# Optimization experiments

Hardware: AMD Instinct MI355X
Metric: run time of the kernel (lower is better)

## Reference

```python
import jax, jax.numpy as jnp
import numpy as np

BATCH = 4
N1 = 131072   # stage-1 voxels (total over batch)
N2 = 32768    # stage-2 (stride-2 downsampled) voxels
D_MODEL = 128
D_INNER = 2 * D_MODEL
D_STATE = 16
D_CONV = 4
DT_RANK = 8   # ceil(d_model / 16)
EPS = 1e-5


def _ln(x, g, b):
    mu = x.mean(-1, keepdims=True)
    v = ((x - mu) ** 2).mean(-1, keepdims=True)
    return (x - mu) * jax.lax.rsqrt(v + EPS) * g + b


def _causal_conv(x, w, b):
    # x: [B,L,Di], w: [Di,K] -> depthwise causal conv1d
    y = jax.lax.conv_general_dilated(
        x.transpose(0, 2, 1), w[:, None, :], (1,), [(D_CONV - 1, 0)],
        dimension_numbers=('NCH', 'OIH', 'NCH'), feature_group_count=D_INNER)
    return y.transpose(0, 2, 1) + b


def _mamba_block(x, ln_g, ln_b, in_w, conv_w, conv_b, xproj_w, dtproj_w, dtproj_b, A_log, Dp, out_w):
    # create_block: LayerNorm -> Mamba mixer (selective scan); returns hidden states
    h = _ln(x, ln_g, ln_b)
    xz = h @ in_w.T                          # [B,L,2*Di]
    xc, z = jnp.split(xz, 2, axis=-1)
    xc = jax.nn.silu(_causal_conv(xc, conv_w, conv_b))
    dbl = xc @ xproj_w.T                     # [B,L,dt_rank+2*d_state]
    dt = jax.nn.softplus(dbl[..., :DT_RANK] @ dtproj_w.T + dtproj_b)  # [B,L,Di]
    Bm = dbl[..., DT_RANK:DT_RANK + D_STATE]
    Cm = dbl[..., DT_RANK + D_STATE:]
    A = -jnp.exp(A_log)                      # [Di,ds]

    def step(hst, inp):
        dt_t, b_t, c_t, u_t = inp            # [B,Di],[B,ds],[B,ds],[B,Di]
        hst = jnp.exp(dt_t[..., None] * A) * hst + (dt_t * u_t)[..., None] * b_t[:, None, :]
        return hst, jnp.einsum('bds,bs->bd', hst, c_t)

    h0 = jnp.zeros((x.shape[0], D_INNER, D_STATE), x.dtype)
    xs = (dt.transpose(1, 0, 2), Bm.transpose(1, 0, 2), Cm.transpose(1, 0, 2), xc.transpose(1, 0, 2))
    _, ys = jax.lax.scan(step, h0, xs)       # ys: [L,B,Di]
    y = ys.transpose(1, 0, 2) + xc * Dp
    y = y * jax.nn.silu(z)
    return y @ out_w.T


def _mamba_params(key):
    ks = jax.random.split(key, 6)
    s = lambda k, sh, sc: jax.random.normal(k, sh, jnp.float32) * sc
    return dict(
        ln_g=jnp.ones((D_MODEL,), jnp.float32), ln_b=jnp.zeros((D_MODEL,), jnp.float32),
        in_w=s(ks[0], (2 * D_INNER, D_MODEL), 0.05),
        conv_w=s(ks[1], (D_INNER, D_CONV), 0.2), conv_b=jnp.zeros((D_INNER,), jnp.float32),
        xproj_w=s(ks[2], (DT_RANK + 2 * D_STATE, D_INNER), 0.05),
        dtproj_w=s(ks[3], (D_INNER, DT_RANK), 0.1), dtproj_b=s(ks[4], (D_INNER,), 0.1),
        A_log=jnp.log(jnp.tile(jnp.arange(1, D_STATE + 1, dtype=jnp.float32), (D_INNER, 1))),
        D=jnp.ones((D_INNER,), jnp.float32),
        out_w=s(ks[5], (D_MODEL, D_INNER), 0.05))


def setup_inputs():
    key = jax.random.key(0)
    k = jax.random.split(key, 10)
    inp = {
        'feats_s1': jax.random.normal(k[0], (N1, D_MODEL), jnp.float32),
        'feats_s2': jax.random.normal(k[1], (N2, D_MODEL), jnp.float32),
        'pos_s1': jax.random.uniform(k[2], (N1, 3), jnp.float32),
        'pos_s2': jax.random.uniform(k[3], (N2, 3), jnp.float32),
        'hilbert_s1': jax.random.randint(k[4], (N1,), 0, 1 << 30, jnp.int32),
        'hilbert_s2': jax.random.randint(k[5], (N2,), 0, 1 << 30, jnp.int32),
        'pe_w': jax.random.normal(k[6], (D_MODEL, 3), jnp.float32) * 0.1,
        'pe_b': jnp.zeros((D_MODEL,), jnp.float32),
        'norm_g': jnp.ones((D_MODEL,), jnp.float32), 'norm_b': jnp.zeros((D_MODEL,), jnp.float32),
        'normb_g': jnp.ones((D_MODEL,), jnp.float32), 'normb_b': jnp.zeros((D_MODEL,), jnp.float32),
    }
    for pref, kk in (('m1_', k[7]), ('m2_', k[8])):
        for n, v in _mamba_params(kk).items():
            inp[pref + n] = v
    return inp


def _forward(feats_s1, feats_s2, pos_s1, pos_s2, pe_w, pe_b, norm_g, norm_b, normb_g, normb_b,
             m1_ln_g, m1_ln_b, m1_in_w, m1_conv_w, m1_conv_b, m1_xproj_w, m1_dtproj_w, m1_dtproj_b, m1_A_log, m1_D, m1_out_w,
             m2_ln_g, m2_ln_b, m2_in_w, m2_conv_w, m2_conv_b, m2_xproj_w, m2_dtproj_w, m2_dtproj_b, m2_A_log, m2_D, m2_out_w,
             hilbert_s1, hilbert_s2):
    L1, L2 = N1 // BATCH, N2 // BATCH
    m1 = (m1_ln_g, m1_ln_b, m1_in_w, m1_conv_w, m1_conv_b, m1_xproj_w, m1_dtproj_w, m1_dtproj_b, m1_A_log, m1_D, m1_out_w)
    m2 = (m2_ln_g, m2_ln_b, m2_in_w, m2_conv_w, m2_conv_b, m2_xproj_w, m2_dtproj_w, m2_dtproj_b, m2_A_log, m2_D, m2_out_w)

    # stage 2: hilbert-order forward scan through mamba_layer1
    f2 = (feats_s2 + pos_s2 @ pe_w.T + pe_b).reshape(BATCH, L2, D_MODEL)
    o2 = jnp.argsort(hilbert_s2.reshape(BATCH, L2), axis=-1)          # inds_curt_to_next
    seq2 = jnp.take_along_axis(f2, o2[..., None], axis=1)
    out2 = _mamba_block(seq2, *m1)
    back2 = jnp.take_along_axis(out2, jnp.argsort(o2, axis=-1)[..., None], axis=1).reshape(N2, D_MODEL)
    out_s2 = _ln(back2, norm_g, norm_b)

    # stage 1: flipped hilbert-order (backward) scan through mamba_layer2
    f1 = (feats_s1 + pos_s1 @ pe_w.T + pe_b).reshape(BATCH, L1, D_MODEL)
    o1 = jnp.argsort(hilbert_s1.reshape(BATCH, L1), axis=-1)
    seq1 = jnp.take_along_axis(f1, o1[..., None], axis=1)[:, ::-1, :]
    out1 = _mamba_block(seq1, *m2)[:, ::-1, :]
    back1 = jnp.take_along_axis(out1, jnp.argsort(o1, axis=-1)[..., None], axis=1).reshape(N1, D_MODEL)
    out_s1 = _ln(back1, normb_g, normb_b)

    return jnp.concatenate([out_s1, out_s2], axis=0)   # [N1+N2, d_model]


def reference(feats_s1, feats_s2, pos_s1, pos_s2, pe_w, pe_b, norm_g, norm_b, normb_g, normb_b,
              m1_ln_g, m1_ln_b, m1_in_w, m1_conv_w, m1_conv_b, m1_xproj_w, m1_dtproj_w, m1_dtproj_b, m1_A_log, m1_D, m1_out_w,
              m2_ln_g, m2_ln_b, m2_in_w, m2_conv_w, m2_conv_b, m2_xproj_w, m2_dtproj_w, m2_dtproj_b, m2_A_log, m2_D, m2_out_w,
              hilbert_s1, hilbert_s2):
    return _forward(feats_s1, feats_s2, pos_s1, pos_s2, pe_w, pe_b, norm_g, norm_b, normb_g, normb_b,
                    m1_ln_g, m1_ln_b, m1_in_w, m1_conv_w, m1_conv_b, m1_xproj_w, m1_dtproj_w, m1_dtproj_b, m1_A_log, m1_D, m1_out_w,
                    m2_ln_g, m2_ln_b, m2_in_w, m2_conv_w, m2_conv_b, m2_xproj_w, m2_dtproj_w, m2_dtproj_b, m2_A_log, m2_D, m2_out_w,
                    hilbert_s1, hilbert_s2)
```

## Files before the change

kernel.cpp:

```cpp
#include <hip/hip_runtime.h>
#include <hip/hip_bf16.h>

#define DEV __device__ __forceinline__

constexpr int BATCH_ = 4;
constexpr int N1_ = 131072;
constexpr int N2_ = 32768;
constexpr int L1_ = N1_ / BATCH_;
constexpr int L2_ = N2_ / BATCH_;
constexpr int DM_ = 128;
constexpr int DI_ = 256;
constexpr int DS_ = 16;
constexpr int DTR_ = 8;
constexpr int TOT_ = N1_ + N2_;

constexpr int TA_ = 32;
constexpr int TAH_ = TA_ + 3;
constexpr int NTILE1_ = L1_ / TA_;
constexpr int NTILE2_ = L2_ / TA_;
constexpr int NTILES_ = 4 * NTILE1_ + 4 * NTILE2_;

constexpr int TS_ = 128;
constexpr int NCH1_ = L1_ / TS_;
constexpr int NCH2_ = L2_ / TS_;
constexpr int NCHUNKS_ = 4 * NCH1_ + 4 * NCH2_;

constexpr int NST_ = 160;

constexpr int IN1_OFF = 0;
constexpr int IN2_OFF = 65536;
constexpr int XP1_OFF = 131072;
constexpr int XP2_OFF = 143360;
constexpr int OW1_OFF = 155648;
constexpr int OW2_OFF = 188416;
constexpr int W16_TOT = 221184;

typedef short short8 __attribute__((ext_vector_type(8)));
typedef float f32x4 __attribute__((ext_vector_type(4)));

struct MP {
  const float* ln_g; const float* ln_b; const float* in_w;
  const float* conv_w; const float* conv_b; const float* xproj_w;
  const float* dtproj_w; const float* dtproj_b; const float* A_log;
  const float* Dp; const float* out_w;
};

DEV float softplusf(float x) {
  return fmaxf(x, 0.f) + __logf(1.f + __expf(-fabsf(x)));
}

DEV unsigned short f2bf(float f) {
  unsigned u = __builtin_bit_cast(unsigned, f);
  u += 0x7fffu + ((u >> 16) & 1u);
  return (unsigned short)(u >> 16);
}
DEV float bf2f(unsigned short s) {
  unsigned u = ((unsigned)s) << 16;
  return __builtin_bit_cast(float, u);
}

DEV void sort_tile_info(int tile, int& seg, int& tis, int& slotbase) {
  if (tile < 128) { seg = tile >> 5; tis = tile & 31; slotbase = seg * L1_; }
  else { seg = 4 + ((tile - 128) >> 3); tis = (tile - 128) & 7; slotbase = N1_ + (seg - 4) * L2_; }
}

__global__ __launch_bounds__(256) void k_prep(
    const float* __restrict__ in_w1, const float* __restrict__ xp1,
    const float* __restrict__ ow1,
    const float* __restrict__ in_w2, const float* __restrict__ xp2,
    const float* __restrict__ ow2,
    unsigned short* __restrict__ w16)
{
  const int i = blockIdx.x * 256 + threadIdx.x;
  if (i >= W16_TOT) return;
  float v;
  if (i < IN2_OFF) v = in_w1[i - IN1_OFF];
  else if (i < XP1_OFF) v = in_w2[i - IN2_OFF];
  else if (i < XP2_OFF) {
    const int j = i - XP1_OFF; const int r = j >> 8;
    v = (r < 40) ? xp1[j] : 0.f;
  } else if (i < OW1_OFF) {
    const int j = i - XP2_OFF; const int r = j >> 8;
    v = (r < 40) ? xp2[j] : 0.f;
  } else if (i < OW2_OFF) v = ow1[i - OW1_OFF];
  else v = ow2[i - OW2_OFF];
  w16[i] = f2bf(v);
}

__global__ __launch_bounds__(256) void k_hist(
    const int* __restrict__ hil1, const int* __restrict__ hil2,
    const unsigned* __restrict__ ksrc, unsigned* __restrict__ histg,
    int shift, int pass0)
{
  const int tile = blockIdx.x;
  int seg, tis, slotbase;
  sort_tile_info(tile, seg, tis, slotbase);
  const int tid = threadIdx.x;
  __shared__ unsigned h[1024];
  #pragma unroll
  for (int i = 0; i < 4; ++i) h[i * 256 + tid] = 0;
  __syncthreads();
  #pragma unroll
  for (int it = 0; it < 4; ++it) {
    const int li = tis * 1024 + it * 256 + tid;
    unsigned k;
    if (pass0) k = (unsigned)(seg < 4 ? hil1[seg * L1_ + li] : hil2[(seg - 4) * L2_ + li]);
    else       k = ksrc[slotbase + li];
    atomicAdd(&h[(k >> shift) & 1023u], 1u);
  }
  __syncthreads();
  #pragma unroll
  for (int i = 0; i < 4; ++i)
    histg[tile * 1024 + i * 256 + tid] = h[i * 256 + tid];
}

__global__ __launch_bounds__(256) void k_scanoff(
    const unsigned* __restrict__ histg, unsigned* __restrict__ offg)
{
  const int seg = blockIdx.x;
  const int ntiles = seg < 4 ? 32 : 8;
  const int tilebase = seg < 4 ? seg * 32 : 128 + (seg - 4) * 8;
  const int tid = threadIdx.x;
  const int d0 = tid * 4;
  unsigned tot[4] = {0, 0, 0, 0};
  for (int t = 0; t < ntiles; ++t) {
    const unsigned* hp = &histg[(size_t)(tilebase + t) * 1024 + d0];
    tot[0] += hp[0]; tot[1] += hp[1]; tot[2] += hp[2]; tot[3] += hp[3];
  }
  unsigned lp[4]; unsigned s = 0;
  #pragma unroll
  for (int j = 0; j < 4; ++j) { lp[j] = s; s += tot[j]; }
  const int lane = tid & 63, wv = tid >> 6;
  unsigned inc = s;
  #pragma unroll
  for (int off = 1; off < 64; off <<= 1) {
    unsigned v = (unsigned)__shfl_up((int)inc, off, 64);
    if (lane >= off) inc += v;
  }
  __shared__ unsigned wsum[4];
  if (lane == 63) wsum[wv] = inc;
  __syncthreads();
  unsigned wbase = 0;
  for (int w = 0; w < 4; ++w) if (w < wv) wbase += wsum[w];
  const unsigned base = wbase + inc - s;
  #pragma unroll
  for (int j = 0; j < 4; ++j) {
    unsigned run = base + lp[j];
    for (int t = 0; t < ntiles; ++t) {
      offg[(size_t)(tilebase + t) * 1024 + d0 + j] = run;
      run += histg[(size_t)(tilebase + t) * 1024 + d0 + j];
    }
  }
}

__global__ __launch_bounds__(256) void k_scatter(
    const int* __restrict__ hil1, const int* __restrict__ hil2,
    const unsigned* __restrict__ ksrc, const int* __restrict__ isrc,
    const unsigned* __restrict__ offg,
    unsigned* __restrict__ kdst, int* __restrict__ idst,
    int* __restrict__ o_all, int shift, int pass0, int last)
{
  const int tile = blockIdx.x;
  int seg, tis, slotbase;
  sort_tile_info(tile, seg, tis, slotbase);
  const int tid = threadIdx.x;
  const int lane = tid & 63, wv = tid >> 6;
  __shared__ unsigned runb[1024];
  __shared__ unsigned wcnt[4 * 1024];
  #pragma unroll
  for (int i = 0; i < 4; ++i) runb[i * 256 + tid] = offg[(size_t)tile * 1024 + i * 256 + tid];
  #pragma unroll
  for (int it = 0; it < 4; ++it) {
    #pragma unroll
    for (int i = 0; i < 16; ++i) wcnt[i * 256 + tid] = 0;
    __syncthreads();
    const int li = tis * 1024 + it * 256 + tid;
    unsigned k; int v;
    if (pass0) {
      k = (unsigned)(seg < 4 ? hil1[seg * L1_ + li] : hil2[(seg - 4) * L2_ + li]);
      v = li;
    } else {
      k = ksrc[slotbase + li]; v = isrc[slotbase + li];
    }
    const unsigned d = (k >> shift) & 1023u;
    unsigned long long m = ~0ull;
    #pragma unroll
    for (int b = 0; b < 10; ++b) {
      const unsigned long long bb = __ballot((int)((d >> b) & 1u));
      m &= ((d >> b) & 1u) ? bb : ~bb;
    }
    const unsigned lrank = (unsigned)__popcll(m & ((1ull << lane) - 1ull));
    wcnt[wv * 1024 + d] = (unsigned)__popcll(m);
    __syncthreads();
    unsigned prior = runb[d];
    for (int w = 0; w < 3; ++w) if (w < wv) prior += wcnt[w * 1024 + d];
    const unsigned pos = prior + lrank;
    if (last) o_all[slotbase + pos] = v;
    else { kdst[slotbase + pos] = k; idst[slotbase + pos] = v; }
    __syncthreads();
    #pragma unroll
    for (int i = 0; i < 4; ++i) {
      const int dd = i * 256 + tid;
      runb[dd] += wcnt[dd] + wcnt[1024 + dd] + wcnt[2048 + dd] + wcnt[3072 + dd];
    }
    __syncthreads();
  }
}

constexpr int HF_ = 132;
constexpr int HB_ = 136;
constexpr int XB_ = 264;
constexpr int OFF_HFP = 18480;
constexpr int OFF_HB16 = 36960;
constexpr int SMEM_A = 50016;

__global__ __launch_bounds__(256) void k_phaseA(
    const float* __restrict__ feats1, const float* __restrict__ feats2,
    const float* __restrict__ pos1, const float* __restrict__ pos2,
    const float* __restrict__ pe_w, const float* __restrict__ pe_b,
    MP p1, MP p2, const int* __restrict__ o_all,
    const unsigned short* __restrict__ w16,
    __hip_bfloat16* __restrict__ xc_g, __hip_bfloat16* __restrict__ z_g,
    float* __restrict__ dbl_g)
{
  const int blk = blockIdx.x;
  bool is1; int b, tile;
  if (blk < 4 * NTILE1_) { is1 = true; b = blk / NTILE1_; tile = blk % NTILE1_; }
  else { const int r = blk - 4 * NTILE1_; is1 = false; b = r / NTILE2_; tile = r % NTILE2_; }
  const int L = is1 ? L1_ : L2_;
  const int slotbase = is1 ? b * L1_ : N1_ + b * L2_;
  const float* feats = is1 ? feats1 + (size_t)b * L1_ * DM_ : feats2 + (size_t)b * L2_ * DM_;
  const float* pos = is1 ? pos1 + (size_t)b * L1_ * 3 : pos2 + (size_t)b * L2_ * 3;
  const MP P = is1 ? p2 : p1;
  const unsigned short* iw16 = w16 + (is1 ? IN2_OFF : IN1_OFF);
  const unsigned short* xp16 = w16 + (is1 ? XP2_OFF : XP1_OFF);
  const bool rev = is1;
  const int t0 = tile * TA_;
  const int pstart = rev ? t0 : t0 - 3;
  const int lsh = rev ? 0 : 3;

  __shared__ char smem[SMEM_A];
  unsigned short* xcb16 = (unsigned short*)smem;
  float* hfp = (float*)(smem + OFF_HFP);
  unsigned short* xc16 = (unsigned short*)(smem + OFF_HFP);
  unsigned short* hb16 = (unsigned short*)(smem + OFF_HB16);

  const int tid = threadIdx.x;
  const int lane = tid & 63, wv = tid >> 6;
  const int l15 = lane & 15, quad = lane >> 4;

  {
    unsigned* hz = (unsigned*)hb16;
    for (int i = tid; i < 48 * HB_ / 2; i += 256) hz[i] = 0;
    const int c = tid & 127;
    const int half = tid >> 7;
    const float pw0 = pe_w[c * 3 + 0], pw1 = pe_w[c * 3 + 1], pw2 = pe_w[c * 3 + 2];
    const float pb = pe_b[c];
    for (int lt = half; lt < TAH_; lt += 2) {
      const int p = pstart + lt;
      if (p >= 0 && p < L) {
        const int orig = o_all[slotbase + p];
        const float* fr = feats + (size_t)orig * DM_;
        const float* pr = pos + (size_t)orig * 3;
        hfp[lt * HF_ + c] = fr[c] + pr[0] * pw0 + pr[1] * pw1 + pr[2] * pw2 + pb;
      }
    }
  }
  __syncthreads();
  {
    for (int lt = wv; lt < TAH_; lt += 4) {
      const int p = pstart + lt;
      if (p < 0 || p >= L) continue;
      float x0 = hfp[lt * HF_ + lane], x1 = hfp[lt * HF_ + lane + 64];
      float s = x0 + x1, q = x0 * x0 + x1 * x1;
      #pragma unroll
      for (int off = 32; off; off >>= 1) {
        s += __shfl_xor(s, off, 64);
        q += __shfl_xor(q, off, 64);
      }
      const float mu = s * (1.f / 128.f);
      const float rs = rsqrtf(q * (1.f / 128.f) - mu * mu + 1e-5f);
      hb16[lt * HB_ + lane]      = f2bf((x0 - mu) * rs * P.ln_g[lane]      + P.ln_b[lane]);
      hb16[lt * HB_ + lane + 64] = f2bf((x1 - mu) * rs * P.ln_g[lane + 64] + P.ln_b[lane + 64]);
    }
  }
  __syncthreads();
  {
    short8 afr[3][4];
    #pragma unroll
    for (int mt = 0; mt < 3; ++mt)
      #pragma unroll
      for (int t = 0; t < 4; ++t)
        afr[mt][t] = *(const short8*)(hb16 + (mt * 16 + l15) * HB_ + t * 32 + quad * 8);
    for (int nn = 0; nn < 8; ++nn) {
      const int ntile = nn * 4 + wv;
      f32x4 acc[3];
      #pragma unroll
      for (int mt = 0; mt < 3; ++mt) acc[mt] = (f32x4){0.f, 0.f, 0.f, 0.f};
      #pragma unroll
      for (int t = 0; t < 4; ++t) {
        const short8 bfr = *(const short8*)(iw16 + (size_t)(ntile * 16 + l15) * DM_ + t * 32 + quad * 8);
        #pragma unroll
        for (int mt = 0; mt < 3; ++mt)
          acc[mt] = __builtin_amdgcn_mfma_f32_16x16x32_bf16(afr[mt][t], bfr, acc[mt], 0, 0, 0);
      }
      const int col = ntile * 16 + l15;
      if (col < 256) {
        #pragma unroll
        for (int mt = 0; mt < 3; ++mt)
          #pragma unroll
          for (int r = 0; r < 4; ++r) {
            const int row = mt * 16 + quad * 4 + r;
            if (row < TAH_) xcb16[row * XB_ + col] = f2bf(acc[mt][r]);
          }
      } else {
        #pragma unroll
        for (int mt = 0; mt < 3; ++mt)
          #pragma unroll
          for (int r = 0; r < 4; ++r) {
            const int row = mt * 16 + quad * 4 + r;
            const int m = row - lsh;
            if (m >= 0 && m < TA_)
              z_g[(size_t)(slotbase + t0 + m) * DI_ + (col - 256)] = __float2bfloat16(acc[mt][r]);
          }
      }
    }
  }
  __syncthreads();
  {
    const int d = tid;
    const float w0 = P.conv_w[d * 4 + 0], w1 = P.conv_w[d * 4 + 1],
                w2 = P.conv_w[d * 4 + 2], w3 = P.conv_w[d * 4 + 3];
    const float cb = P.conv_b[d];
    float x0 = bf2f(xcb16[0 * XB_ + d]), x1 = bf2f(xcb16[1 * XB_ + d]),
          x2 = bf2f(xcb16[2 * XB_ + d]);
    unsigned short out16[TA_];
    #pragma unroll
    for (int m = 0; m < TA_; ++m) {
      const float x3 = bf2f(xcb16[(m + 3) * XB_ + d]);
      float v;
      if (rev) v = w3 * x0 + w2 * x1 + w1 * x2 + w0 * x3;
      else     v = w0 * x0 + w1 * x1 + w2 * x2 + w3 * x3;
      v += cb;
      v = v * (1.f / (1.f + __expf(-v)));
      const unsigned short vb = f2bf(v);
      out16[m] = vb;
      xc_g[(size_t)(slotbase + t0 + m) * DI_ + d] = __builtin_bit_cast(__hip_bfloat16, vb);
      x0 = x1; x1 = x2; x2 = x3;
    }
    __syncthreads();
    #pragma unroll
    for (int m = 0; m < TA_; ++m) xc16[m * XB_ + d] = out16[m];
  }
  __syncthreads();
  if (wv < 3) {
    f32x4 acc0 = (f32x4){0.f,0.f,0.f,0.f}, acc1 = acc0;
    #pragma unroll
    for (int t = 0; t < 8; ++t) {
      const short8 bfr = *(const short8*)(xp16 + (size_t)(wv * 16 + l15) * DI_ + t * 32 + quad * 8);
      const short8 a0 = *(const short8*)(xc16 + (l15) * XB_ + t * 32 + quad * 8);
      const short8 a1 = *(const short8*)(xc16 + (16 + l15) * XB_ + t * 32 + quad * 8);
      acc0 = __builtin_amdgcn_mfma_f32_16x16x32_bf16(a0, bfr, acc0, 0, 0, 0);
      acc1 = __builtin_amdgcn_mfma_f32_16x16x32_bf16(a1, bfr, acc1, 0, 0, 0);
    }
    const int col = wv * 16 + l15;
    if (col < 40) {
      #pragma unroll
      for (int r = 0; r < 4; ++r) {
        dbl_g[(size_t)(slotbase + t0 + quad * 4 + r) * 40 + col] = acc0[r];
        dbl_g[(size_t)(slotbase + t0 + 16 + quad * 4 + r) * 40 + col] = acc1[r];
      }
    }
  }
}

struct ScanP {
  float Av[DS_]; float A0; bool fast;
  float dtw[DTR_]; float dtb;
};
DEV void load_scanp(const MP& P, int d, ScanP& sp) {
  #pragma unroll
  for (int s = 0; s < DS_; ++s) sp.Av[s] = -__expf(P.A_log[d * DS_ + s]);
  sp.A0 = sp.Av[0];
  bool f = true;
  #pragma unroll
  for (int s = 0; s < DS_; ++s)
    f = f && (fabsf(sp.Av[s] - (float)(s + 1) * sp.A0) <= 1e-3f * (float)(s + 1));
  sp.fast = f;
  #pragma unroll
  for (int r = 0; r < DTR_; ++r) sp.dtw[r] = P.dtproj_w[d * DTR_ + r];
  sp.dtb = P.dtproj_b[d];
}
DEV float dt_from(const float4& q0, const float4& q1, const ScanP& sp) {
  const float dtraw = sp.dtb
      + q0.x*sp.dtw[0] + q0.y*sp.dtw[1] + q0.z*sp.dtw[2] + q0.w*sp.dtw[3]
      + q1.x*sp.dtw[4] + q1.y*sp.dtw[5] + q1.z*sp.dtw[6] + q1.w*sp.dtw[7];
  return softplusf(dtraw);
}

__global__ __launch_bounds__(256) void k_scan1(
    MP p1, MP p2,
    const __hip_bfloat16* __restrict__ xc_g, const float* __restrict__ dbl_g,
    float* __restrict__ hloc, float* __restrict__ sumdt_g)
{
  const int blk = blockIdx.x;
  bool is1; int b, pc;
  if (blk < 4 * NCH1_) { is1 = true; b = blk / NCH1_; pc = blk % NCH1_; }
  else { const int r = blk - 4 * NCH1_; is1 = false; b = r / NCH2_; pc = r % NCH2_; }
  const MP P = is1 ? p2 : p1;
  const int L = is1 ? L1_ : L2_;
  const bool rev = is1;
  const int slotbase = is1 ? b * L1_ : N1_ + b * L2_;
  const int d = threadIdx.x;
  ScanP sp; load_scanp(P, d, sp);
  const unsigned short* xcp = (const unsigned short*)xc_g;
  float h[DS_];
  #pragma unroll
  for (int s = 0; s < DS_; ++s) h[s] = 0.f;
  float sdt = 0.f;
  const int s0 = rev ? (L - (pc + 1) * TS_) : pc * TS_;
  const int dp = rev ? -1 : 1;
  int slot = slotbase + (rev ? (s0 + TS_ - 1) : s0);
  if (sp.fast) {
    const float* dr = dbl_g + (size_t)slot * 40;
    float4 q0 = *(const float4*)dr, q1 = *(const float4*)(dr + 4);
    float4 Bv[4];
    #pragma unroll
    for (int j = 0; j < 4; ++j) Bv[j] = *(const float4*)(dr + 8 + 4 * j);
    float u = bf2f(xcp[(size_t)slot * DI_ + d]);
    for (int i = 0; i < TS_; ++i) {
      const int nslot = (i + 1 < TS_) ? slot + dp : slot;
      const float* nr = dbl_g + (size_t)nslot * 40;
      float4 nq0 = *(const float4*)nr, nq1 = *(const float4*)(nr + 4);
      float4 nB[4];
      #pragma unroll
      for (int j = 0; j < 4; ++j) nB[j] = *(const float4*)(nr + 8 + 4 * j);
      const float nu = bf2f(xcp[(size_t)nslot * DI_ + d]);
      const float dt = dt_from(q0, q1, sp);
      const float du = dt * u;
      sdt += dt;
      const float e1 = __expf(dt * sp.A0);
      const float e2 = e1 * e1, e3 = e2 * e1, e4 = e2 * e2;
      float base = 1.f;
      #pragma unroll
      for (int j = 0; j < 4; ++j) {
        const float m1 = base * e1, m2 = base * e2, m3 = base * e3, m4 = base * e4;
        h[4*j+0] = m1 * h[4*j+0] + du * Bv[j].x;
        h[4*j+1] = m2 * h[4*j+1] + du * Bv[j].y;
        h[4*j+2] = m3 * h[4*j+2] + du * Bv[j].z;
        h[4*j+3] = m4 * h[4*j+3] + du * Bv[j].w;
        base = m4;
      }
      slot = nslot; q0 = nq0; q1 = nq1; u = nu;
      #pragma unroll
      for (int j = 0; j < 4; ++j) Bv[j] = nB[j];
    }
  } else {
    for (int i = 0; i < TS_; ++i) {
      const float* dr = dbl_g + (size_t)slot * 40;
      const float4 q0 = *(const float4*)dr, q1 = *(const float4*)(dr + 4);
      const float dt = dt_from(q0, q1, sp);
      const float u = bf2f(xcp[(size_t)slot * DI_ + d]);
      const float du = dt * u;
      sdt += dt;
      float Bvv[16];
      #pragma unroll
      for (int j = 0; j < 4; ++j) *(float4*)&Bvv[4*j] = *(const float4*)(dr + 8 + 4*j);
      #pragma unroll
      for (int s = 0; s < DS_; ++s)
        h[s] = __expf(dt * sp.Av[s]) * h[s] + du * Bvv[s];
      slot += dp;
    }
  }
  float* hl = hloc + (size_t)blk * DS_ * DI_;
  #pragma unroll
  for (int s = 0; s < DS_; ++s) hl[s * DI_ + d] = h[s];
  sumdt_g[(size_t)blk * DI_ + d] = sdt;
}

__global__ __launch_bounds__(256) void k_scan2(
    MP p1, MP p2, const float* __restrict__ hloc,
    const float* __restrict__ sumdt_g, float* __restrict__ hin)
{
  const int seq = blockIdx.x >> 4;
  const int s = blockIdx.x & 15;
  const bool is1 = seq < 4;
  const int b = is1 ? seq : seq - 4;
  const MP P = is1 ? p2 : p1;
  const int nch = is1 ? NCH1_ : NCH2_;
  const int chbase = is1 ? b * NCH1_ : 4 * NCH1_ + b * NCH2_;
  const int d = threadIdx.x;
  const float A = -__expf(P.A_log[d * DS_ + s]);
  float carry = 0.f;
  for (int pc = 0; pc < nch; ++pc) {
    const size_t idx = (size_t)(chbase + pc);
    const float sdt = sumdt_g[idx * DI_ + d];
    hin[idx * DS_ * DI_ + s * DI_ + d] = carry;
    carry = __expf(A * sdt) * carry + hloc[idx * DS_ * DI_ + s * DI_ + d];
  }
}

__global__ __launch_bounds__(256) void k_scan3(
    MP p1, MP p2,
    const __hip_bfloat16* __restrict__ xc_g, const float* __restrict__ dbl_g,
    const float* __restrict__ hin, __hip_bfloat16* zv_g)
{
  const int blk = blockIdx.x;
  bool is1; int b, pc;
  if (blk < 4 * NCH1_) { is1 = true; b = blk / NCH1_; pc = blk % NCH1_; }
  else { const int r = blk - 4 * NCH1_; is1 = false; b = r / NCH2_; pc = r % NCH2_; }
  const MP P = is1 ? p2 : p1;
  const int L = is1 ? L1_ : L2_;
  const bool rev = is1;
  const int slotbase = is1 ? b * L1_ : N1_ + b * L2_;
  const int d = threadIdx.x;
  ScanP sp; load_scanp(P, d, sp);
  const float Dp = P.Dp[d];
  const unsigned short* xcp = (const unsigned short*)xc_g;
  unsigned short* zvp = (unsigned short*)zv_g;
  float h[DS_];
  const float* hi = hin + (size_t)blk * DS_ * DI_;
  #pragma unroll
  for (int s = 0; s < DS_; ++s) h[s] = hi[s * DI_ + d];
  const int s0 = rev ? (L - (pc + 1) * TS_) : pc * TS_;
  const int dp = rev ? -1 : 1;
  int slot = slotbase + (rev ? (s0 + TS_ - 1) : s0);
  if (sp.fast) {
    const float* dr = dbl_g + (size_t)slot * 40;
    float4 q0 = *(const float4*)dr, q1 = *(const float4*)(dr + 4);
    float4 Bv[4], Cv[4];
    #pragma unroll
    for (int j = 0; j < 4; ++j) {
      Bv[j] = *(const float4*)(dr + 8 + 4 * j);
      Cv[j] = *(const float4*)(dr + 24 + 4 * j);
    }
    float u = bf2f(xcp[(size_t)slot * DI_ + d]);
    float zv = bf2f(zvp[(size_t)slot * DI_ + d]);
    for (int i = 0; i < TS_; ++i) {
      const int nslot = (i + 1 < TS_) ? slot + dp : slot;
      const float* nr = dbl_g + (size_t)nslot * 40;
      float4 nq0 = *(const float4*)nr, nq1 = *(const float4*)(nr + 4);
      float4 nB[4], nC[4];
      #pragma unroll
      for (int j = 0; j < 4; ++j) {
        nB[j] = *(const float4*)(nr + 8 + 4 * j);
        nC[j] = *(const float4*)(nr + 24 + 4 * j);
      }
      const float nu = bf2f(xcp[(size_t)nslot * DI_ + d]);
      const float nz = bf2f(zvp[(size_t)nslot * DI_ + d]);
      const float dt = dt_from(q0, q1, sp);
      const float du = dt * u;
      const float e1 = __expf(dt * sp.A0);
      const float e2 = e1 * e1, e3 = e2 * e1, e4 = e2 * e2;
      float base = 1.f;
      float y = 0.f;
      #pragma unroll
      for (int j = 0; j < 4; ++j) {
        const float m1 = base * e1, m2 = base * e2, m3 = base * e3, m4 = base * e4;
        h[4*j+0] = m1 * h[4*j+0] + du * Bv[j].x;  y += h[4*j+0] * Cv[j].x;
        h[4*j+1] = m2 * h[4*j+1] + du * Bv[j].y;  y += h[4*j+1] * Cv[j].y;
        h[4*j+2] = m3 * h[4*j+2] + du * Bv[j].z;  y += h[4*j+2] * Cv[j].z;
        h[4*j+3] = m4 * h[4*j+3] + du * Bv[j].w;  y += h[4*j+3] * Cv[j].w;
        base = m4;
      }
      const float sg = zv / (1.f + __expf(-zv));
      zvp[(size_t)slot * DI_ + d] = f2bf((y + u * Dp) * sg);
      slot = nslot; q0 = nq0; q1 = nq1; u = nu; zv = nz;
      #pragma unroll
      for (int j = 0; j < 4; ++j) { Bv[j] = nB[j]; Cv[j] = nC[j]; }
    }
  } else {
    for (int i = 0; i < TS_; ++i) {
      const float* dr = dbl_g + (size_t)slot * 40;
      const float4 q0 = *(const float4*)dr, q1 = *(const float4*)(dr + 4);
      const float dt = dt_from(q0, q1, sp);
      const float u = bf2f(xcp[(size_t)slot * DI_ + d]);
      const float zv = bf2f(zvp[(size_t)slot * DI_ + d]);
      const float du = dt * u;
      float Bvv[16], Cvv[16];
      #pragma unroll
      for (int j = 0; j < 4; ++j) {
        *(float4*)&Bvv[4*j] = *(const float4*)(dr + 8 + 4*j);
        *(float4*)&Cvv[4*j] = *(const float4*)(dr + 24 + 4*j);
      }
      float y = 0.f;
      #pragma unroll
      for (int s = 0; s < DS_; ++s) {
        h[s] = __expf(dt * sp.Av[s]) * h[s] + du * Bvv[s];
        y += h[s] * Cvv[s];
      }
      const float sg = zv / (1.f + __expf(-zv));
      zvp[(size_t)slot * DI_ + d] = f2bf((y + u * Dp) * sg);
      slot += dp;
    }
  }
}

constexpr int OB_ = 132;
__global__ __launch_bounds__(256) void k_final(
    const __hip_bfloat16* __restrict__ v_g, const int* __restrict__ o_all,
    const unsigned short* __restrict__ w16,
    const float* __restrict__ norm_g, const float* __restrict__ norm_b,
    const float* __restrict__ normb_g, const float* __restrict__ normb_b,
    float* __restrict__ out)
{
  const int blk = blockIdx.x;
  bool is1; int b, tile;
  if (blk < 4 * NTILE1_) { is1 = true; b = blk / NTILE1_; tile = blk % NTILE1_; }
  else { const int r = blk - 4 * NTILE1_; is1 = false; b = r / NTILE2_; tile = r % NTILE2_; }
  const unsigned short* W = w16 + (is1 ? OW2_OFF : OW1_OFF);
  const float* gg = is1 ? normb_g : norm_g;
  const float* gb = is1 ? normb_b : norm_b;
  const int slotbase = is1 ? b * L1_ : N1_ + b * L2_;
  const int t0 = tile * TA_;
  __shared__ unsigned short v16[TA_ * XB_];
  __shared__ float obuf[TA_ * OB_];
  const int tid = threadIdx.x;
  const int lane = tid & 63, wv = tid >> 6;
  const int l15 = lane & 15, quad = lane >> 4;
  {
    const int c2 = tid & 127;
    const int half = tid >> 7;
    const unsigned short* vp = (const unsigned short*)v_g;
    for (int m = half * 16; m < half * 16 + 16; ++m) {
      const unsigned* src = (const unsigned*)(vp + (size_t)(slotbase + t0 + m) * DI_);
      ((unsigned*)&v16[m * XB_])[c2] = src[c2];
    }
  }
  __syncthreads();
  for (int nn = 0; nn < 2; ++nn) {
    const int ntile = wv + nn * 4;
    f32x4 acc0 = (f32x4){0.f,0.f,0.f,0.f}, acc1 = acc0;
    #pragma unroll
    for (int t = 0; t < 8; ++t) {
      const short8 bfr = *(const short8*)(W + (size_t)(ntile * 16 + l15) * DI_ + t * 32 + quad * 8);
      const short8 a0 = *(const short8*)(v16 + (l15) * XB_ + t * 32 + quad * 8);
      const short8 a1 = *(const short8*)(v16 + (16 + l15) * XB_ + t * 32 + quad * 8);
      acc0 = __builtin_amdgcn_mfma_f32_16x16x32_bf16(a0, bfr, acc0, 0, 0, 0);
      acc1 = __builtin_amdgcn_mfma_f32_16x16x32_bf16(a1, bfr, acc1, 0, 0, 0);
    }
    const int col = ntile * 16 + l15;
    #pragma unroll
    for (int r = 0; r < 4; ++r) {
      obuf[(quad * 4 + r) * OB_ + col] = acc0[r];
      obuf[(16 + quad * 4 + r) * OB_ + col] = acc1[r];
    }
  }
  __syncthreads();
  {
    for (int m = wv; m < TA_; m += 4) {
      float x0 = obuf[m * OB_ + lane], x1 = obuf[m * OB_ + lane + 64];
      float s = x0 + x1, q = x0 * x0 + x1 * x1;
      #pragma unroll
      for (int off = 32; off; off >>= 1) {
        s += __shfl_xor(s, off, 64);
        q += __shfl_xor(q, off, 64);
      }
      const float mu = s * (1.f / 128.f);
      const float rs = rsqrtf(q * (1.f / 128.f) - mu * mu + 1e-5f);
      const int orig = o_all[slotbase + t0 + m];
      float* orow = out + (size_t)(slotbase + orig) * DM_;
      orow[lane]      = (x0 - mu) * rs * gg[lane]      + gb[lane];
      orow[lane + 64] = (x1 - mu) * rs * gg[lane + 64] + gb[lane + 64];
    }
  }
}

extern "C" void kernel_launch(void* const* d_in, const int* in_sizes, int n_in,
                              void* d_out, int out_size, void* d_ws, size_t ws_size,
                              hipStream_t stream)
{
  (void)in_sizes; (void)n_in; (void)out_size; (void)ws_size;
  const float* feats1 = (const float*)d_in[0];
  const float* feats2 = (const float*)d_in[1];
  const float* pos1   = (const float*)d_in[2];
  const float* pos2   = (const float*)d_in[3];
  const int*   hil1   = (const int*)d_in[4];
  const int*   hil2   = (const int*)d_in[5];
  const float* pe_w   = (const float*)d_in[6];
  const float* pe_b   = (const float*)d_in[7];
  const float* norm_g  = (const float*)d_in[8];
  const float* norm_b  = (const float*)d_in[9];
  const float* normb_g = (const float*)d_in[10];
  const float* normb_b = (const float*)d_in[11];
  MP p1 { (const float*)d_in[12], (const float*)d_in[13], (const float*)d_in[14],
          (const float*)d_in[15], (const float*)d_in[16], (const float*)d_in[17],
          (const float*)d_in[18], (const float*)d_in[19], (const float*)d_in[20],
          (const float*)d_in[21], (const float*)d_in[22] };
  MP p2 { (const float*)d_in[23], (const float*)d_in[24], (const float*)d_in[25],
          (const float*)d_in[26], (const float*)d_in[27], (const float*)d_in[28],
          (const float*)d_in[29], (const float*)d_in[30], (const float*)d_in[31],
          (const float*)d_in[32], (const float*)d_in[33] };

  char* w = (char*)d_ws;
  auto take = [&](size_t bytes) -> char* {
    char* p = w; w += (bytes + 255) & ~(size_t)255; return p;
  };
  int* o_all = (int*)take((size_t)TOT_ * 4);
  unsigned* kA = (unsigned*)take((size_t)TOT_ * 4);
  int* iA = (int*)take((size_t)TOT_ * 4);
  unsigned* kB = (unsigned*)take((size_t)TOT_ * 4);
  int* iB = (int*)take((size_t)TOT_ * 4);
  unsigned* histg = (unsigned*)take((size_t)NST_ * 1024 * 4);
  unsigned* offg  = (unsigned*)take((size_t)NST_ * 1024 * 4);
  __hip_bfloat16* xc = (__hip_bfloat16*)take((size_t)TOT_ * DI_ * 2);
  __hip_bfloat16* vzb = (__hip_bfloat16*)take((size_t)TOT_ * DI_ * 2);
  float* dbl = (float*)take((size_t)TOT_ * 40 * 4);
  float* hloc = (float*)take((size_t)NCHUNKS_ * DS_ * DI_ * 4);
  float* hin  = (float*)take((size_t)NCHUNKS_ * DS_ * DI_ * 4);
  float* sdt  = (float*)take((size_t)NCHUNKS_ * DI_ * 4);
  unsigned short* w16 = (unsigned short*)take((size_t)W16_TOT * 2);

  hipLaunchKernelGGL(k_prep, dim3((W16_TOT + 255) / 256), dim3(256), 0, stream,
                     p1.in_w, p1.xproj_w, p1.out_w, p2.in_w, p2.xproj_w, p2.out_w, w16);
  hipLaunchKernelGGL(k_hist, dim3(NST_), dim3(256), 0, stream,
                     hil1, hil2, kB, histg, 0, 1);
  hipLaunchKernelGGL(k_scanoff, dim3(8), dim3(256), 0, stream, histg, offg);
  hipLaunchKernelGGL(k_scatter, dim3(NST_), dim3(256), 0, stream,
                     hil1, hil2, kB, iB, offg, kB, iB, o_all, 0, 1, 0);
  hipLaunchKernelGGL(k_hist, dim3(NST_), dim3(256), 0, stream,
                     hil1, hil2, kB, histg, 10, 0);
  hipLaunchKernelGGL(k_scanoff, dim3(8), dim3(256), 0, stream, histg, offg);
  hipLaunchKernelGGL(k_scatter, dim3(NST_), dim3(256), 0, stream,
                     hil1, hil2, kB, iB, offg, kA, iA, o_all, 10, 0, 0);
  hipLaunchKernelGGL(k_hist, dim3(NST_), dim3(256), 0, stream,
                     hil1, hil2, kA, histg, 20, 0);
  hipLaunchKernelGGL(k_scanoff, dim3(8), dim3(256), 0, stream, histg, offg);
  hipLaunchKernelGGL(k_scatter, dim3(NST_), dim3(256), 0, stream,
                     hil1, hil2, kA, iA, offg, kB, iB, o_all, 20, 0, 1);

  hipLaunchKernelGGL(k_phaseA, dim3(NTILES_), dim3(256), 0, stream,
                     feats1, feats2, pos1, pos2, pe_w, pe_b, p1, p2, o_all, w16,
                     xc, vzb, dbl);
  hipLaunchKernelGGL(k_scan1, dim3(NCHUNKS_), dim3(256), 0, stream,
                     p1, p2, xc, dbl, hloc, sdt);
  hipLaunchKernelGGL(k_scan2, dim3(128), dim3(256), 0, stream,
                     p1, p2, hloc, sdt, hin);
  hipLaunchKernelGGL(k_scan3, dim3(NCHUNKS_), dim3(256), 0, stream,
                     p1, p2, xc, dbl, hin, vzb);
  hipLaunchKernelGGL(k_final, dim3(NTILES_), dim3(256), 0, stream,
                     vzb, o_all, w16, norm_g, norm_b, normb_g, normb_b,
                     (float*)d_out);
}
```

Before: 952.7 us.

## Fuse pos-embed with LayerNorm in registers, shrink phaseA smem, load final GEMM operands directly

In k_phaseA the positional-embedding add and the input LayerNorm now run per wave in registers, so the fp32 staging buffer and one barrier are gone and shared memory shrinks. Only the padding rows of the bf16 tile are zeroed now, since every real row is written directly. The conv output is written back in place into the same shared buffer, dropping the register array and an extra sync. k_final now reads MFMA A fragments straight from global memory instead of staging them in LDS, and each wave computes two N tiles at once. The smaller LDS footprint may raise occupancy, at the cost of redundant, less coalesced global reads in k_final.

```diff
diff --git a/kernel.cpp b/kernel.cpp
--- a/kernel.cpp
+++ b/kernel.cpp
@@ -207,12 +207,10 @@
   }
 }
 
-constexpr int HF_ = 132;
 constexpr int HB_ = 136;
 constexpr int XB_ = 264;
-constexpr int OFF_HFP = 18480;
-constexpr int OFF_HB16 = 36960;
-constexpr int SMEM_A = 50016;
+constexpr int OFF_HB16 = TAH_ * XB_ * 2;
+constexpr int SMEM_A = OFF_HB16 + 48 * HB_ * 2;
 
 __global__ __launch_bounds__(256) void k_phaseA(
     const float* __restrict__ feats1, const float* __restrict__ feats2,
@@ -241,9 +239,8 @@
 
   __shared__ char smem[SMEM_A];
   unsigned short* xcb16 = (unsigned short*)smem;
-  float* hfp = (float*)(smem + OFF_HFP);
-  unsigned short* xc16 = (unsigned short*)(smem + OFF_HFP);
   unsigned short* hb16 = (unsigned short*)(smem + OFF_HB16);
+  unsigned short* xc16 = xcb16;
 
   const int tid = threadIdx.x;
   const int lane = tid & 63, wv = tid >> 6;
@@ -251,37 +248,40 @@
 
   {
     unsigned* hz = (unsigned*)hb16;
-    for (int i = tid; i < 48 * HB_ / 2; i += 256) hz[i] = 0;
-    const int c = tid & 127;
-    const int half = tid >> 7;
-    const float pw0 = pe_w[c * 3 + 0], pw1 = pe_w[c * 3 + 1], pw2 = pe_w[c * 3 + 2];
-    const float pb = pe_b[c];
-    for (int lt = half; lt < TAH_; lt += 2) {
+    for (int i = tid; i < 13 * (HB_ / 2); i += 256)
+      hz[TAH_ * (HB_ / 2) + i] = 0;
+    const float pw00 = pe_w[lane * 3 + 0], pw01 = pe_w[lane * 3 + 1], pw02 = pe_w[lane * 3 + 2];
+    const float pw10 = pe_w[(lane + 64) * 3 + 0], pw11 = pe_w[(lane + 64) * 3 + 1],
+                pw12 = pe_w[(lane + 64) * 3 + 2];
+    const float pb0 = pe_b[lane], pb1 = pe_b[lane + 64];
+    const float g0 = P.ln_g[lane], g1 = P.ln_g[lane + 64];
+    const float bt0 = P.ln_b[lane], bt1 = P.ln_b[lane + 64];
+    #pragma unroll
+    for (int k = 0; k < 9; ++k) {
+      const int lt = wv + k * 4;
+      if (lt >= TAH_) break;
       const int p = pstart + lt;
+      unsigned short o0 = 0, o1 = 0;
       if (p >= 0 && p < L) {
         const int orig = o_all[slotbase + p];
         const float* fr = feats + (size_t)orig * DM_;
         const float* pr = pos + (size_t)orig * 3;
-        hfp[lt * HF_ + c] = fr[c] + pr[0] * pw0 + pr[1] * pw1 + pr[2] * pw2 + pb;
-      }
-    }
-  }
-  __syncthreads();
-  {
-    for (int lt = wv; lt < TAH_; lt += 4) {
-      const int p = pstart + lt;
-      if (p < 0 || p >= L) continue;
-      float x0 = hfp[lt * HF_ + lane], x1 = hfp[lt * HF_ + lane + 64];
-      float s = x0 + x1, q = x0 * x0 + x1 * x1;
-      #pragma unroll
-      for (int off = 32; off; off >>= 1) {
-        s += __shfl_xor(s, off, 64);
-        q += __shfl_xor(q, off, 64);
-      }
-      const float mu = s * (1.f / 128.f);
-      const float rs = rsqrtf(q * (1.f / 128.f) - mu * mu + 1e-5f);
-      hb16[lt * HB_ + lane]      = f2bf((x0 - mu) * rs * P.ln_g[lane]      + P.ln_b[lane]);
-      hb16[lt * HB_ + lane + 64] = f2bf((x1 - mu) * rs * P.ln_g[lane + 64] + P.ln_b[lane + 64]);
+        const float c0 = pr[0], c1 = pr[1], c2 = pr[2];
+        float x0 = fr[lane]      + c0 * pw00 + c1 * pw01 + c2 * pw02 + pb0;
+        float x1 = fr[lane + 64] + c0 * pw10 + c1 * pw11 + c2 * pw12 + pb1;
+        float s = x0 + x1, q = x0 * x0 + x1 * x1;
+        #pragma unroll
+        for (int off = 32; off; off >>= 1) {
+          s += __shfl_xor(s, off, 64);
+          q += __shfl_xor(q, off, 64);
+        }
+        const float mu = s * (1.f / 128.f);
+        const float rs = rsqrtf(q * (1.f / 128.f) - mu * mu + 1e-5f);
+        o0 = f2bf((x0 - mu) * rs * g0 + bt0);
+        o1 = f2bf((x1 - mu) * rs * g1 + bt1);
+      }
+      hb16[lt * HB_ + lane]      = o0;
+      hb16[lt * HB_ + lane + 64] = o1;
     }
   }
   __syncthreads();
@@ -334,7 +334,6 @@
     const float cb = P.conv_b[d];
     float x0 = bf2f(xcb16[0 * XB_ + d]), x1 = bf2f(xcb16[1 * XB_ + d]),
           x2 = bf2f(xcb16[2 * XB_ + d]);
-    unsigned short out16[TA_];
     #pragma unroll
     for (int m = 0; m < TA_; ++m) {
       const float x3 = bf2f(xcb16[(m + 3) * XB_ + d]);
@@ -344,13 +343,10 @@
       v += cb;
       v = v * (1.f / (1.f + __expf(-v)));
       const unsigned short vb = f2bf(v);
-      out16[m] = vb;
       xc_g[(size_t)(slotbase + t0 + m) * DI_ + d] = __builtin_bit_cast(__hip_bfloat16, vb);
+      xcb16[m * XB_ + d] = vb;
       x0 = x1; x1 = x2; x2 = x3;
     }
-    __syncthreads();
-    #pragma unroll
-    for (int m = 0; m < TA_; ++m) xc16[m * XB_ + d] = out16[m];
   }
   __syncthreads();
   if (wv < 3) {
@@ -613,37 +609,32 @@
   const float* gb = is1 ? normb_b : norm_b;
   const int slotbase = is1 ? b * L1_ : N1_ + b * L2_;
   const int t0 = tile * TA_;
-  __shared__ unsigned short v16[TA_ * XB_];
   __shared__ float obuf[TA_ * OB_];
   const int tid = threadIdx.x;
   const int lane = tid & 63, wv = tid >> 6;
   const int l15 = lane & 15, quad = lane >> 4;
   {
-    const int c2 = tid & 127;
-    const int half = tid >> 7;
-    const unsigned short* vp = (const unsigned short*)v_g;
-    for (int m = half * 16; m < half * 16 + 16; ++m) {
-      const unsigned* src = (const unsigned*)(vp + (size_t)(slotbase + t0 + m) * DI_);
-      ((unsigned*)&v16[m * XB_])[c2] = src[c2];
-    }
-  }
-  __syncthreads();
-  for (int nn = 0; nn < 2; ++nn) {
-    const int ntile = wv + nn * 4;
-    f32x4 acc0 = (f32x4){0.f,0.f,0.f,0.f}, acc1 = acc0;
+    const unsigned short* vp = (const unsigned short*)v_g + (size_t)(slotbase + t0) * DI_;
+    f32x4 acc00 = (f32x4){0.f,0.f,0.f,0.f}, acc01 = acc00, acc10 = acc00, acc11 = acc00;
     #pragma unroll
     for (int t = 0; t < 8; ++t) {
-      const short8 bfr = *(const short8*)(W + (size_t)(ntile * 16 + l15) * DI_ + t * 32 + quad * 8);
-      const short8 a0 = *(const short8*)(v16 + (l15) * XB_ + t * 32 + quad * 8);
-      const short8 a1 = *(const short8*)(v16 + (16 + l15) * XB_ + t * 32 + quad * 8);
-      acc0 = __builtin_amdgcn_mfma_f32_16x16x32_bf16(a0, bfr, acc0, 0, 0, 0);
-      acc1 = __builtin_amdgcn_mfma_f32_16x16x32_bf16(a1, bfr, acc1, 0, 0, 0);
-    }
-    const int col = ntile * 16 + l15;
+      const short8 a0 = *(const short8*)(vp + (size_t)(l15) * DI_ + t * 32 + quad * 8);
+      const short8 a1 = *(const short8*)(vp + (size_t)(16 + l15) * DI_ + t * 32 + quad * 8);
+      const short8 b0 = *(const short8*)(W + (size_t)((wv) * 16 + l15) * DI_ + t * 32 + quad * 8);
+      const short8 b1 = *(const short8*)(W + (size_t)((wv + 4) * 16 + l15) * DI_ + t * 32 + quad * 8);
+      acc00 = __builtin_amdgcn_mfma_f32_16x16x32_bf16(a0, b0, acc00, 0, 0, 0);
+      acc01 = __builtin_amdgcn_mfma_f32_16x16x32_bf16(a1, b0, acc01, 0, 0, 0);
+      acc10 = __builtin_amdgcn_mfma_f32_16x16x32_bf16(a0, b1, acc10, 0, 0, 0);
+      acc11 = __builtin_amdgcn_mfma_f32_16x16x32_bf16(a1, b1, acc11, 0, 0, 0);
+    }
+    const int col0 = wv * 16 + l15;
+    const int col1 = (wv + 4) * 16 + l15;
     #pragma unroll
     for (int r = 0; r < 4; ++r) {
-      obuf[(quad * 4 + r) * OB_ + col] = acc0[r];
-      obuf[(16 + quad * 4 + r) * OB_ + col] = acc1[r];
+      obuf[(quad * 4 + r) * OB_ + col0] = acc00[r];
+      obuf[(16 + quad * 4 + r) * OB_ + col0] = acc01[r];
+      obuf[(quad * 4 + r) * OB_ + col1] = acc10[r];
+      obuf[(16 + quad * 4 + r) * OB_ + col1] = acc11[r];
     }
   }
   __syncthreads();
```

Measured after the change: 887.6 us. 6.8% less time.
